# Optimization experiments

Measured on AMD Instinct MI355X. Metric: run time of the kernel, lower is better.

Reference implementation:

```python
import jax, jax.numpy as jnp
import numpy as np

N_NODES = 50000
N_EDGES = 1600000
N_GRAPHS = 512
IN_DIM = 384
HID = 128


def gcn_conv(x, W, b, src, dst, n_nodes):
    # PyG GCNConv: h = W^T x, then propagate with sym norm over A + I (self-loops).
    h = x @ W  # [N, out]
    # self-loops
    loop = jnp.arange(n_nodes, dtype=src.dtype)
    s = jnp.concatenate([src, loop])
    d = jnp.concatenate([dst, loop])
    ones = jnp.ones(s.shape[0], dtype=h.dtype)
    deg = jax.ops.segment_sum(ones, d, num_segments=n_nodes)  # in-degree incl self-loop
    dis = jnp.where(deg > 0, jax.lax.rsqrt(deg), 0.0)
    norm = dis[s] * dis[d]  # [E+N]
    msg = h[s] * norm[:, None]  # gather + scale
    out = jax.ops.segment_sum(msg, d, num_segments=n_nodes)  # scatter-add
    return out + b


def global_mean_pool(x, batch, num_graphs):
    sums = jax.ops.segment_sum(x, batch, num_segments=num_graphs)
    cnt = jax.ops.segment_sum(jnp.ones(x.shape[0], dtype=x.dtype), batch, num_segments=num_graphs)
    return sums / jnp.maximum(cnt, 1.0)[:, None]


def setup_inputs() -> dict:
    key = jax.random.key(0)
    ks = jax.random.split(key, 12)
    x = jax.random.normal(ks[0], (N_NODES, IN_DIM), dtype=jnp.float32)
    edge_index = jax.random.randint(ks[1], (2, N_EDGES), 0, N_NODES, dtype=jnp.int64 if jax.config.jax_enable_x64 else jnp.int32)
    batch = jnp.sort(jax.random.randint(ks[2], (N_NODES,), 0, N_GRAPHS, dtype=jnp.int32))
    def glorot(k, shape):
        lim = float(np.sqrt(6.0 / (shape[0] + shape[1])))
        return jax.random.uniform(k, shape, jnp.float32, -lim, lim)
    return {
        "x": x,
        "edge_index": edge_index,
        "batch": batch,
        "W1": glorot(ks[3], (IN_DIM, HID)),
        "b1": jnp.zeros((HID,), jnp.float32),
        "W2": glorot(ks[4], (HID, HID)),
        "b2": jnp.zeros((HID,), jnp.float32),
        "Wl1": glorot(ks[5], (HID, HID // 2)),
        "bl1": jnp.zeros((HID // 2,), jnp.float32),
        "Wl2": glorot(ks[6], (HID // 2, 5)),
        "bl2": jnp.zeros((5,), jnp.float32),
    }


def reference(x, edge_index, batch, W1, b1, W2, b2, Wl1, bl1, Wl2, bl2):
    src, dst = edge_index[0], edge_index[1]
    n = x.shape[0]
    h = jax.nn.relu(gcn_conv(x, W1, b1, src, dst, n))
    h = jax.nn.relu(gcn_conv(h, W2, b2, src, dst, n))
    g = global_mean_pool(h, batch, N_GRAPHS)  # [G, HID]
    g = jax.nn.relu(g @ Wl1 + bl1)
    return jax.nn.sigmoid(g @ Wl2 + bl2)  # [G, 5]
```

## Files before the change

kernel.cpp:

```cpp
#include <hip/hip_runtime.h>
#include <hip/hip_bf16.h>

#define HID 128
#define NGRAPH 512
#define IN_DIM 384

typedef __attribute__((ext_vector_type(2))) float f32x2;

__global__ void deg_kernel(const int* __restrict__ dst, int* __restrict__ deg, int E) {
    int e = blockIdx.x * blockDim.x + threadIdx.x;
    if (e < E) atomicAdd(&deg[dst[e]], 1);
}

__global__ void dis_kernel(const int* __restrict__ deg, float* __restrict__ dis, int n) {
    int v = blockIdx.x * blockDim.x + threadIdx.x;
    if (v < n) dis[v] = rsqrtf((float)(deg[v] + 1));
}

__global__ __launch_bounds__(256) void scan_part(const int* __restrict__ deg, int* __restrict__ row,
                                                 int* __restrict__ blockSums, int n) {
    __shared__ int ts[256];
    const int b = blockIdx.x, t = threadIdx.x;
    const int base = b * 1024 + t * 4;
    int v0 = (base + 0 < n) ? deg[base + 0] : 0;
    int v1 = (base + 1 < n) ? deg[base + 1] : 0;
    int v2 = (base + 2 < n) ? deg[base + 2] : 0;
    int v3 = (base + 3 < n) ? deg[base + 3] : 0;
    const int s = v0 + v1 + v2 + v3;
    ts[t] = s;
    __syncthreads();
    for (int off = 1; off < 256; off <<= 1) {
        int x = (t >= off) ? ts[t - off] : 0;
        __syncthreads();
        ts[t] += x;
        __syncthreads();
    }
    int p = ts[t] - s;
    if (base + 0 < n) { row[base + 0] = p; p += v0; }
    if (base + 1 < n) { row[base + 1] = p; p += v1; }
    if (base + 2 < n) { row[base + 2] = p; p += v2; }
    if (base + 3 < n) { row[base + 3] = p; }
    if (t == 255) blockSums[b] = ts[255];
}

__global__ void scan_tops(int* __restrict__ blockSums, int nb) {
    if (threadIdx.x == 0 && blockIdx.x == 0) {
        int acc = 0;
        for (int i = 0; i < nb; i++) { int v = blockSums[i]; blockSums[i] = acc; acc += v; }
    }
}

__global__ __launch_bounds__(256) void scan_add(int* __restrict__ row, int* __restrict__ cursor,
                                                const int* __restrict__ blockSums, int n, int E) {
    const int b = blockIdx.x, t = threadIdx.x;
    const int off = blockSums[b];
    const int base = b * 1024 + t * 4;
#pragma unroll
    for (int j = 0; j < 4; j++) {
        int i = base + j;
        if (i < n) { int v = row[i] + off; row[i] = v; cursor[i] = v; }
    }
    if (b == 0 && t == 0) row[n] = E;
}

__global__ void fill_kernel(const int* __restrict__ src, const int* __restrict__ dst,
                            int* __restrict__ cursor, unsigned short* __restrict__ csr16,
                            int E, int lo, int hi) {
    int e = blockIdx.x * blockDim.x + threadIdx.x;
    if (e < E) {
        const int d = dst[e];
        if (d >= lo && d < hi) {
            int pos = atomicAdd(&cursor[d], 1);
            csr16[pos] = (unsigned short)src[e];
        }
    }
}

template <int K>
__global__ __launch_bounds__(256) void gemm_tile(const float* __restrict__ X,
                                                 const float* __restrict__ W,
                                                 const float* __restrict__ dis,
                                                 unsigned int* __restrict__ out8, int n) {
    constexpr int KC = 32;
    __shared__ float asT[KC][68];
    __shared__ float bs[KC * HID];
    const int t = threadIdx.x;
    const int tx = t & 31;
    const int ty = t >> 5;
    const int row0 = blockIdx.x * 64;

    float4 acc[8];
#pragma unroll
    for (int j = 0; j < 8; j++) acc[j] = make_float4(0.f, 0.f, 0.f, 0.f);

    const int ar = t >> 3;
    const int af = t & 7;

    for (int k0 = 0; k0 < K; k0 += KC) {
#pragma unroll
        for (int half = 0; half < 2; half++) {
            const int r = ar + half * 32;
            const int gr = row0 + r;
            float4 a = make_float4(0.f, 0.f, 0.f, 0.f);
            if (gr < n) a = *(const float4*)&X[(long)gr * K + k0 + af * 4];
            asT[af * 4 + 0][r] = a.x;
            asT[af * 4 + 1][r] = a.y;
            asT[af * 4 + 2][r] = a.z;
            asT[af * 4 + 3][r] = a.w;
        }
        {
            const float4* wp = (const float4*)&W[(long)k0 * HID];
            float4* bp = (float4*)bs;
#pragma unroll
            for (int i = 0; i < 4; i++) bp[t + i * 256] = wp[t + i * 256];
        }
        __syncthreads();
#pragma unroll 8
        for (int kk = 0; kk < KC; kk++) {
            const float4 a0 = *(const float4*)&asT[kk][ty * 8];
            const float4 a1 = *(const float4*)&asT[kk][ty * 8 + 4];
            const float4 b  = *(const float4*)&bs[kk * HID + tx * 4];
            acc[0].x = fmaf(a0.x, b.x, acc[0].x); acc[0].y = fmaf(a0.x, b.y, acc[0].y);
            acc[0].z = fmaf(a0.x, b.z, acc[0].z); acc[0].w = fmaf(a0.x, b.w, acc[0].w);
            acc[1].x = fmaf(a0.y, b.x, acc[1].x); acc[1].y = fmaf(a0.y, b.y, acc[1].y);
            acc[1].z = fmaf(a0.y, b.z, acc[1].z); acc[1].w = fmaf(a0.y, b.w, acc[1].w);
            acc[2].x = fmaf(a0.z, b.x, acc[2].x); acc[2].y = fmaf(a0.z, b.y, acc[2].y);
            acc[2].z = fmaf(a0.z, b.z, acc[2].z); acc[2].w = fmaf(a0.z, b.w, acc[2].w);
            acc[3].x = fmaf(a0.w, b.x, acc[3].x); acc[3].y = fmaf(a0.w, b.y, acc[3].y);
            acc[3].z = fmaf(a0.w, b.z, acc[3].z); acc[3].w = fmaf(a0.w, b.w, acc[3].w);
            acc[4].x = fmaf(a1.x, b.x, acc[4].x); acc[4].y = fmaf(a1.x, b.y, acc[4].y);
            acc[4].z = fmaf(a1.x, b.z, acc[4].z); acc[4].w = fmaf(a1.x, b.w, acc[4].w);
            acc[5].x = fmaf(a1.y, b.x, acc[5].x); acc[5].y = fmaf(a1.y, b.y, acc[5].y);
            acc[5].z = fmaf(a1.y, b.z, acc[5].z); acc[5].w = fmaf(a1.y, b.w, acc[5].w);
            acc[6].x = fmaf(a1.z, b.x, acc[6].x); acc[6].y = fmaf(a1.z, b.y, acc[6].y);
            acc[6].z = fmaf(a1.z, b.z, acc[6].z); acc[6].w = fmaf(a1.z, b.w, acc[6].w);
            acc[7].x = fmaf(a1.w, b.x, acc[7].x); acc[7].y = fmaf(a1.w, b.y, acc[7].y);
            acc[7].z = fmaf(a1.w, b.z, acc[7].z); acc[7].w = fmaf(a1.w, b.w, acc[7].w);
        }
        __syncthreads();
    }

#pragma unroll
    for (int j = 0; j < 8; j++) {
        const int v = row0 + ty * 8 + j;
        if (v < n) {
            const float s = dis[v] * 8.0f;
            int w01 = __builtin_amdgcn_cvt_pk_fp8_f32(acc[j].x * s, acc[j].y * s, 0, false);
            int w   = __builtin_amdgcn_cvt_pk_fp8_f32(acc[j].z * s, acc[j].w * s, w01, true);
            out8[(long)v * (HID / 4) + tx] = (unsigned int)w;
        }
    }
}

template <bool POOL>
__global__ __launch_bounds__(256) void agg_kernel(const unsigned char* __restrict__ hs8,
                                                  const unsigned short* __restrict__ csr16,
                                                  const int* __restrict__ row,
                                                  const float* __restrict__ dis,
                                                  const float* __restrict__ bias,
                                                  const int* __restrict__ batch,
                                                  float* __restrict__ buf,
                                                  float* __restrict__ sums,
                                                  int* __restrict__ cnt, int n) {
    const int v = blockIdx.x * 4 + (threadIdx.x >> 6);
    if (v >= n) return;
    const int lane = threadIdx.x & 63;
    const int sub = lane >> 3;
    const int lc  = lane & 7;

    const int rs = row[v];
    const int re = row[v + 1];

    const int col = (lc << 4) + (sub << 1);
    const unsigned short selfw = *(const unsigned short*)&hs8[(long)v * HID + col];
    const float dv = dis[v] * 0.125f;
    const float bx = bias[col];
    const float by = bias[col + 1];
    int g = 0;
    if (POOL) g = batch[v];

    float acc[16];
#pragma unroll
    for (int i = 0; i < 16; i++) acc[i] = 0.f;

    for (int base = rs; base < re; base += 64) {
        int ei = base + lane;
        if (ei >= re) ei = re - 1;
        const int myidx = (int)__builtin_nontemporal_load(&csr16[ei]);

        uint4 w[8];
#pragma unroll
        for (int p = 0; p < 8; p++) {
            const int pe = base + p * 8;
            if (pe < re) {
                const int idx = __shfl(myidx, p * 8 + sub, 64);
                w[p] = *(const uint4*)&hs8[(long)idx * HID + (lc << 4)];
            } else {
                w[p] = make_uint4(0u, 0u, 0u, 0u);
            }
        }
#pragma unroll
        for (int p = 0; p < 8; p++) {
            if (base + p * 8 + sub < re) {
                const uint4 ww = w[p];
                f32x2 u;
                u = __builtin_amdgcn_cvt_pk_f32_fp8(ww.x, false); acc[0]  += u.x; acc[1]  += u.y;
                u = __builtin_amdgcn_cvt_pk_f32_fp8(ww.x, true);  acc[2]  += u.x; acc[3]  += u.y;
                u = __builtin_amdgcn_cvt_pk_f32_fp8(ww.y, false); acc[4]  += u.x; acc[5]  += u.y;
                u = __builtin_amdgcn_cvt_pk_f32_fp8(ww.y, true);  acc[6]  += u.x; acc[7]  += u.y;
                u = __builtin_amdgcn_cvt_pk_f32_fp8(ww.z, false); acc[8]  += u.x; acc[9]  += u.y;
                u = __builtin_amdgcn_cvt_pk_f32_fp8(ww.z, true);  acc[10] += u.x; acc[11] += u.y;
                u = __builtin_amdgcn_cvt_pk_f32_fp8(ww.w, false); acc[12] += u.x; acc[13] += u.y;
                u = __builtin_amdgcn_cvt_pk_f32_fp8(ww.w, true);  acc[14] += u.x; acc[15] += u.y;
            }
        }
    }

#pragma unroll
    for (int i = 0; i < 16; i++) {
        acc[i] += __shfl_xor(acc[i], 8, 64);
        acc[i] += __shfl_xor(acc[i], 16, 64);
        acc[i] += __shfl_xor(acc[i], 32, 64);
    }

    f32x2 sf = __builtin_amdgcn_cvt_pk_f32_fp8((unsigned int)selfw, false);
    const float sx = acc[(sub << 1) + 0] + sf.x;
    const float sy = acc[(sub << 1) + 1] + sf.y;
    const float rx = fmaxf(fmaf(dv, sx, bx), 0.f);
    const float ry = fmaxf(fmaf(dv, sy, by), 0.f);
    if (POOL) {
        unsafeAtomicAdd(&sums[g * HID + col], rx);
        unsafeAtomicAdd(&sums[g * HID + col + 1], ry);
        if (lane == 0) atomicAdd(&cnt[g], 1);
    } else {
        float2 r; r.x = rx; r.y = ry;
        *(float2*)&buf[(long)v * HID + col] = r;
    }
}

__global__ __launch_bounds__(64) void mlp_kernel(const float* __restrict__ sums,
                                                 const int* __restrict__ cnt,
                                                 const float* __restrict__ Wl1,
                                                 const float* __restrict__ bl1,
                                                 const float* __restrict__ Wl2,
                                                 const float* __restrict__ bl2,
                                                 float* __restrict__ out) {
    const int g = blockIdx.x, t = threadIdx.x;
    __shared__ float mean[HID];
    __shared__ float hid[64];
    const float c = fmaxf((float)cnt[g], 1.0f);
    mean[t] = sums[g * HID + t] / c;
    mean[t + 64] = sums[g * HID + 64 + t] / c;
    __syncthreads();
    float acc = bl1[t];
#pragma unroll 4
    for (int k = 0; k < HID; k++) acc = fmaf(mean[k], Wl1[k * 64 + t], acc);
    hid[t] = fmaxf(acc, 0.f);
    __syncthreads();
    if (t < 5) {
        float a = bl2[t];
#pragma unroll 4
        for (int k = 0; k < 64; k++) a = fmaf(hid[k], Wl2[k * 5 + t], a);
        out[g * 5 + t] = 1.f / (1.f + expf(-a));
    }
}

extern "C" void kernel_launch(void* const* d_in, const int* in_sizes, int n_in,
                              void* d_out, int out_size, void* d_ws, size_t ws_size,
                              hipStream_t stream) {
    const float* x   = (const float*)d_in[0];
    const int* ei    = (const int*)d_in[1];
    const int* batch = (const int*)d_in[2];
    const float* W1  = (const float*)d_in[3];
    const float* b1  = (const float*)d_in[4];
    const float* W2  = (const float*)d_in[5];
    const float* b2  = (const float*)d_in[6];
    const float* Wl1 = (const float*)d_in[7];
    const float* bl1 = (const float*)d_in[8];
    const float* Wl2 = (const float*)d_in[9];
    const float* bl2 = (const float*)d_in[10];
    float* out = (float*)d_out;

    const int n = in_sizes[0] / IN_DIM;
    const int E = in_sizes[1] / 2;
    const int* src = ei;
    const int* dst = ei + E;

    char* ws = (char*)d_ws;
    size_t off = 0;
    auto alloc = [&](size_t bytes) {
        void* p = ws + off;
        off = (off + bytes + 255) & ~(size_t)255;
        return p;
    };
    int*   deg       = (int*)alloc((size_t)n * 4);
    float* dis       = (float*)alloc((size_t)n * 4);
    int*   row       = (int*)alloc((size_t)(n + 1) * 4);
    int*   cursor    = (int*)alloc((size_t)n * 4);
    unsigned short* csr16 = (unsigned short*)alloc((size_t)E * 2);
    int*   blockSums = (int*)alloc(256 * 4);
    unsigned char* hs8 = (unsigned char*)alloc((size_t)n * HID);
    float* buf1 = (float*)alloc((size_t)n * HID * 4);
    float* sums = (float*)alloc((size_t)NGRAPH * HID * 4);
    int*   cnt  = (int*)alloc((size_t)NGRAPH * 4);
    (void)ws_size;

    const int nb = (n + 1023) / 1024;
    const int gemmBlocks = (n + 63) / 64;
    const int aggBlocks  = (n + 3) / 4;
    const int edgeBlocks = (E + 255) / 256;

    hipMemsetAsync(deg, 0, (size_t)n * 4, stream);
    deg_kernel<<<edgeBlocks, 256, 0, stream>>>(dst, deg, E);
    dis_kernel<<<(n + 255) / 256, 256, 0, stream>>>(deg, dis, n);
    scan_part<<<nb, 256, 0, stream>>>(deg, row, blockSums, n);
    scan_tops<<<1, 64, 0, stream>>>(blockSums, nb);
    scan_add<<<nb, 256, 0, stream>>>(row, cursor, blockSums, n, E);
    {
        const int step = (n + 3) / 4;
        for (int k = 0; k < 4; k++) {
            const int lo = k * step;
            const int hi = (k == 3) ? n : (lo + step);
            fill_kernel<<<edgeBlocks, 256, 0, stream>>>(src, dst, cursor, csr16, E, lo, hi);
        }
    }

    gemm_tile<IN_DIM><<<gemmBlocks, 256, 0, stream>>>(x, W1, dis, (unsigned int*)hs8, n);
    agg_kernel<false><<<aggBlocks, 256, 0, stream>>>(hs8, csr16, row, dis, b1, batch,
                                                     buf1, nullptr, nullptr, n);

    gemm_tile<HID><<<gemmBlocks, 256, 0, stream>>>(buf1, W2, dis, (unsigned int*)hs8, n);
    hipMemsetAsync(sums, 0, (size_t)NGRAPH * HID * 4, stream);
    hipMemsetAsync(cnt, 0, (size_t)NGRAPH * 4, stream);
    agg_kernel<true><<<aggBlocks, 256, 0, stream>>>(hs8, csr16, row, dis, b2, batch,
                                                    nullptr, sums, cnt, n);

    mlp_kernel<<<NGRAPH, 64, 0, stream>>>(sums, cnt, Wl1, bl1, Wl2, bl2, out);
}
```

Measured before the change: 591.7 us.

## Process two nodes per wavefront in aggregation, 32 lanes per node

The aggregation kernel now assigns two destination nodes to each 64-lane wavefront, one per half-wave. Each half processes edges in windows of 32, and both halves run the larger of their two window counts. With about 33 edges per node on average, this is meant to cut the lanes left idle when a node's edge list is much shorter than 64. The cost is divergence between the two halves, since the shorter one idles while the longer finishes. It also adds one fewer shuffle-reduction step and wider 4-element epilogue stores and atomics.

New measurement: 653.8 us. 1.1x slower.

```diff
diff --git a/kernel.cpp b/kernel.cpp
--- a/kernel.cpp
+++ b/kernel.cpp
@@ -162,20 +162,26 @@
                                                   float* __restrict__ buf,
                                                   float* __restrict__ sums,
                                                   int* __restrict__ cnt, int n) {
-    const int v = blockIdx.x * 4 + (threadIdx.x >> 6);
-    if (v >= n) return;
+    const int wave = threadIdx.x >> 6;
     const int lane = threadIdx.x & 63;
-    const int sub = lane >> 3;
-    const int lc  = lane & 7;
+    const int h    = lane >> 5;
+    const int l32  = lane & 31;
+    const int sub  = l32 >> 3;
+    const int lc   = l32 & 7;
+
+    const int vb = blockIdx.x * 8 + wave * 2;
+    if (vb >= n) return;
+    int v = vb + h;
+    const bool vok = (v < n);
+    if (!vok) v = n - 1;
 
     const int rs = row[v];
     const int re = row[v + 1];
 
-    const int col = (lc << 4) + (sub << 1);
-    const unsigned short selfw = *(const unsigned short*)&hs8[(long)v * HID + col];
+    const int col = (lc << 4) + (sub << 2);
+    const unsigned int selfw = *(const unsigned int*)&hs8[(long)v * HID + col];
     const float dv = dis[v] * 0.125f;
-    const float bx = bias[col];
-    const float by = bias[col + 1];
+    const float4 bq = *(const float4*)&bias[col];
     int g = 0;
     if (POOL) g = batch[v];
 
@@ -183,17 +189,22 @@
 #pragma unroll
     for (int i = 0; i < 16; i++) acc[i] = 0.f;
 
-    for (int base = rs; base < re; base += 64) {
-        int ei = base + lane;
-        if (ei >= re) ei = re - 1;
+    int win = (re - rs + 31) >> 5;
+    { int other = __shfl_xor(win, 32, 64); win = win > other ? win : other; }
+    const int last = (re > rs) ? (re - 1) : 0;
+
+    for (int wnd = 0; wnd < win; ++wnd) {
+        const int base = rs + (wnd << 5);
+        int ei = base + l32;
+        if (ei > last) ei = last;
         const int myidx = (int)__builtin_nontemporal_load(&csr16[ei]);
 
         uint4 w[8];
 #pragma unroll
         for (int p = 0; p < 8; p++) {
-            const int pe = base + p * 8;
+            const int pe = base + (p << 2);
             if (pe < re) {
-                const int idx = __shfl(myidx, p * 8 + sub, 64);
+                const int idx = __shfl(myidx, h * 32 + (p << 2) + sub, 64);
                 w[p] = *(const uint4*)&hs8[(long)idx * HID + (lc << 4)];
             } else {
                 w[p] = make_uint4(0u, 0u, 0u, 0u);
@@ -201,7 +212,7 @@
         }
 #pragma unroll
         for (int p = 0; p < 8; p++) {
-            if (base + p * 8 + sub < re) {
+            if (base + (p << 2) + sub < re) {
                 const uint4 ww = w[p];
                 f32x2 u;
                 u = __builtin_amdgcn_cvt_pk_f32_fp8(ww.x, false); acc[0]  += u.x; acc[1]  += u.y;
@@ -220,21 +231,26 @@
     for (int i = 0; i < 16; i++) {
         acc[i] += __shfl_xor(acc[i], 8, 64);
         acc[i] += __shfl_xor(acc[i], 16, 64);
-        acc[i] += __shfl_xor(acc[i], 32, 64);
-    }
-
-    f32x2 sf = __builtin_amdgcn_cvt_pk_f32_fp8((unsigned int)selfw, false);
-    const float sx = acc[(sub << 1) + 0] + sf.x;
-    const float sy = acc[(sub << 1) + 1] + sf.y;
-    const float rx = fmaxf(fmaf(dv, sx, bx), 0.f);
-    const float ry = fmaxf(fmaf(dv, sy, by), 0.f);
-    if (POOL) {
-        unsafeAtomicAdd(&sums[g * HID + col], rx);
-        unsafeAtomicAdd(&sums[g * HID + col + 1], ry);
-        if (lane == 0) atomicAdd(&cnt[g], 1);
-    } else {
-        float2 r; r.x = rx; r.y = ry;
-        *(float2*)&buf[(long)v * HID + col] = r;
+    }
+
+    f32x2 s01 = __builtin_amdgcn_cvt_pk_f32_fp8(selfw, false);
+    f32x2 s23 = __builtin_amdgcn_cvt_pk_f32_fp8(selfw, true);
+    const float r0 = fmaxf(fmaf(dv, acc[(sub << 2) + 0] + s01.x, bq.x), 0.f);
+    const float r1 = fmaxf(fmaf(dv, acc[(sub << 2) + 1] + s01.y, bq.y), 0.f);
+    const float r2 = fmaxf(fmaf(dv, acc[(sub << 2) + 2] + s23.x, bq.z), 0.f);
+    const float r3 = fmaxf(fmaf(dv, acc[(sub << 2) + 3] + s23.y, bq.w), 0.f);
+
+    if (vok) {
+        if (POOL) {
+            unsafeAtomicAdd(&sums[g * HID + col + 0], r0);
+            unsafeAtomicAdd(&sums[g * HID + col + 1], r1);
+            unsafeAtomicAdd(&sums[g * HID + col + 2], r2);
+            unsafeAtomicAdd(&sums[g * HID + col + 3], r3);
+            if (l32 == 0) atomicAdd(&cnt[g], 1);
+        } else {
+            float4 r; r.x = r0; r.y = r1; r.z = r2; r.w = r3;
+            *(float4*)&buf[(long)v * HID + col] = r;
+        }
     }
 }
 
@@ -307,7 +323,7 @@
 
     const int nb = (n + 1023) / 1024;
     const int gemmBlocks = (n + 63) / 64;
-    const int aggBlocks  = (n + 3) / 4;
+    const int aggBlocks  = (n + 7) / 8;
     const int edgeBlocks = (E + 255) / 256;
 
     hipMemsetAsync(deg, 0, (size_t)n * 4, stream);
```
